# Optimization experiments

Hardware: AMD Instinct MI355X
Metric: run time of the kernel (lower is better)

Reference implementation:

```python
import jax, jax.numpy as jnp
import numpy as np

NUM_HEADS = 16
LN_EPS = 1e-5


def _layer_norm(x, w, b):
    mean = jnp.mean(x, axis=-1, keepdims=True)
    xc = x - mean
    var = jnp.mean(xc * xc, axis=-1, keepdims=True)
    return xc * jax.lax.rsqrt(var + LN_EPS) * w + b


def _triton_softmax(a):
    # Faithful to TritonSoftmax: clamp to [-100,100], stable softmax with
    # +1e-6 in the denominator, then +1e-8 and renormalize.
    a = jnp.clip(a, -100.0, 100.0)
    a = a - jnp.max(a, axis=-1, keepdims=True)
    e = jnp.exp(a)
    p = e / (jnp.sum(e, axis=-1, keepdims=True) + 1e-6)
    p = p + 1e-8
    return p / jnp.sum(p, axis=-1, keepdims=True)


def _triton_gelu(x):
    # y = 0.5*x*(1 + u/(1+|u|)) with u = x * sqrt(2/pi)*(1+0.044715*x^2)
    coeff = 0.7978845608028654 * (1.0 + 0.044715 * x * x)
    u = x * coeff
    return 0.5 * x * (1.0 + u / (1.0 + jnp.abs(u)))


def setup_inputs() -> dict:
    key = jax.random.key(0)
    ks = jax.random.split(key, 6)
    B, T, D = 2, 2048, 1024
    s = 0.02
    return {
        "x": jax.random.normal(ks[0], (B, T, D), jnp.float32),
        "ln1_w": jnp.ones((D,), jnp.float32),
        "ln1_b": jnp.zeros((D,), jnp.float32),
        "ln2_w": jnp.ones((D,), jnp.float32),
        "ln2_b": jnp.zeros((D,), jnp.float32),
        "w_qkv": jax.random.normal(ks[1], (D, 3 * D), jnp.float32) * s,
        "w_proj": jax.random.normal(ks[2], (D, D), jnp.float32) * s,
        "w_ff1": jax.random.normal(ks[3], (D, 4 * D), jnp.float32) * s,
        "w_ff2": jax.random.normal(ks[4], (4 * D, D), jnp.float32) * s,
    }


def reference(x, ln1_w, ln1_b, ln2_w, ln2_b, w_qkv, w_proj, w_ff1, w_ff2):
    B, T, D = x.shape
    H = NUM_HEADS
    hd = D // H
    scale = hd ** -0.5

    # ---- attention sublayer (pre-LN) ----
    h = _layer_norm(x, ln1_w, ln1_b)
    qkv = (h @ w_qkv).reshape(B, T, 3, H, hd).transpose(2, 0, 3, 1, 4)
    q, k, v = qkv[0], qkv[1], qkv[2]  # [B,H,T,hd]
    attn = jnp.einsum("bhqd,bhkd->bhqk", q, k) * scale  # [B,H,T,T]
    causal = jnp.tril(jnp.ones((T, T), bool))
    attn = jnp.where(causal, attn, -jnp.inf)
    attn = _triton_softmax(attn)  # dropout is identity at eval
    o = jnp.einsum("bhqk,bhkd->bhqd", attn, v)
    o = o.transpose(0, 2, 1, 3).reshape(B, T, D)
    x = x + o @ w_proj

    # ---- MLP sublayer (pre-LN) ----
    h = _layer_norm(x, ln2_w, ln2_b)
    x = x + _triton_gelu(h @ w_ff1) @ w_ff2
    return x
```

## Files before the change

kernel.cpp:

```cpp
#include <hip/hip_runtime.h>

typedef __attribute__((ext_vector_type(8))) __bf16 bf16x8;
typedef __attribute__((ext_vector_type(8))) unsigned short u16x8;
typedef __attribute__((ext_vector_type(4))) unsigned short u16x4;
typedef __attribute__((ext_vector_type(4))) float f32x4;

__device__ __forceinline__ unsigned short f2bf(float f) {
  return __builtin_bit_cast(unsigned short, (__bf16)f);
}

__device__ __forceinline__ bf16x8 ldb8(const unsigned short* p) {
  u16x8 u = *(const u16x8*)p;
  return __builtin_bit_cast(bf16x8, u);
}

__device__ __forceinline__ f32x4 mfma16(bf16x8 a, bf16x8 b, f32x4 c) {
  return __builtin_amdgcn_mfma_f32_16x16x32_bf16(a, b, c, 0, 0, 0);
}

__device__ __forceinline__ void gload16(const void* g, void* l) {
  __builtin_amdgcn_global_load_lds(
      (const __attribute__((address_space(1))) void*)g,
      (__attribute__((address_space(3))) void*)l, 16, 0, 0);
}

__device__ __forceinline__ float gelu_t(float x) {
  float u = x * (0.7978845608028654f * (1.0f + 0.044715f * x * x));
  return 0.5f * x * (1.0f + u / (1.0f + fabsf(u)));
}

__global__ __launch_bounds__(256) void tconv_kernel(const float* __restrict__ in,
                                                    unsigned short* __restrict__ out,
                                                    int R, int C) {
  __shared__ unsigned short tile[64][68];
  int r0 = blockIdx.y * 64, c0 = blockIdx.x * 64;
  int tx = threadIdx.x & 63, tg = threadIdx.x >> 6;
  for (int rr = tg; rr < 64; rr += 4)
    tile[tx][rr] = f2bf(in[(size_t)(r0 + rr) * C + c0 + tx]);
  __syncthreads();
  for (int cc = tg; cc < 64; cc += 4)
    out[(size_t)(c0 + cc) * R + r0 + tx] = tile[cc][tx];
}

__global__ __launch_bounds__(256) void vtrans_kernel(const unsigned short* __restrict__ V,
                                                     unsigned short* __restrict__ VT) {
  __shared__ unsigned short tile[64][68];
  int bh = blockIdx.y;
  int t0 = blockIdx.x * 64;
  const unsigned short* in = V + (size_t)bh * 2048 * 64;
  unsigned short* out = VT + (size_t)bh * 64 * 2048;
  int tx = threadIdx.x & 63, tg = threadIdx.x >> 6;
  for (int rr = tg; rr < 64; rr += 4)
    tile[tx][rr] = in[(size_t)(t0 + rr) * 64 + tx];
  __syncthreads();
  for (int dd = tg; dd < 64; dd += 4)
    out[(size_t)dd * 2048 + t0 + tx] = tile[dd][tx];
}

__global__ __launch_bounds__(256) void ln_kernel(const float* __restrict__ X,
                                                 const float* __restrict__ W,
                                                 const float* __restrict__ Bv,
                                                 unsigned short* __restrict__ H) {
  int row = blockIdx.x;
  int t = threadIdx.x;
  float4 v = ((const float4*)(X + (size_t)row * 1024))[t];
  float s = v.x + v.y + v.z + v.w;
  float s2 = v.x * v.x + v.y * v.y + v.z * v.z + v.w * v.w;
#pragma unroll
  for (int m = 32; m >= 1; m >>= 1) { s += __shfl_xor(s, m); s2 += __shfl_xor(s2, m); }
  __shared__ float red[8];
  if ((t & 63) == 0) { red[t >> 6] = s; red[4 + (t >> 6)] = s2; }
  __syncthreads();
  s = red[0] + red[1] + red[2] + red[3];
  s2 = red[4] + red[5] + red[6] + red[7];
  float mean = s * (1.f / 1024.f);
  float var = fmaxf(s2 * (1.f / 1024.f) - mean * mean, 0.f);
  float rs = rsqrtf(var + 1e-5f);
  float4 w4 = ((const float4*)W)[t];
  float4 b4 = ((const float4*)Bv)[t];
  u16x4 o;
  o[0] = f2bf((v.x - mean) * rs * w4.x + b4.x);
  o[1] = f2bf((v.y - mean) * rs * w4.y + b4.y);
  o[2] = f2bf((v.z - mean) * rs * w4.z + b4.z);
  o[3] = f2bf((v.w - mean) * rs * w4.w + b4.w);
  *(u16x4*)(H + (size_t)row * 1024 + t * 4) = o;
}

template <int MODE, bool DBUF>
__global__ __launch_bounds__(256) void gemm_kernel(
    const unsigned short* __restrict__ A, const unsigned short* __restrict__ B,
    const float* __restrict__ RES, void* __restrict__ OUT,
    unsigned short* __restrict__ Qo, unsigned short* __restrict__ Ko,
    unsigned short* __restrict__ Vo, int M, int N, int K) {
  __shared__ __align__(16) unsigned short As[DBUF ? 2 : 1][128 * 64];
  __shared__ __align__(16) unsigned short Bs[DBUF ? 2 : 1][128 * 64];
  const int tid = threadIdx.x;
  const int lane = tid & 63;
  const int wid = __builtin_amdgcn_readfirstlane(tid >> 6);
  const int lane16 = lane & 15, lgrp = lane >> 4;
  const int l8 = lane >> 3;
  const int lb = (lane & 7) * 16;
  const int m0 = blockIdx.y * 128, n0 = blockIdx.x * 128;
  const int wr = wid >> 1, wc = wid & 1;

  f32x4 acc[4][4] = {};

  const char* Ab = (const char*)A + (size_t)m0 * K * 2;
  const char* Bb = (const char*)B + (size_t)n0 * K * 2;
  const size_t rs = (size_t)K * 2;

  auto stage = [&](int k0, int b) {
#pragma unroll
    for (int i = 0; i < 4; ++i) {
      int c = wid * 4 + i;
      gload16(Ab + (size_t)(c * 8 + l8) * rs + (size_t)k0 * 2 + lb,
              (char*)&As[0][0] + b * 16384 + c * 1024);
      gload16(Bb + (size_t)(c * 8 + l8) * rs + (size_t)k0 * 2 + lb,
              (char*)&Bs[0][0] + b * 16384 + c * 1024);
    }
  };

  const int kIt = K / 64;
  if (DBUF) stage(0, 0);

  for (int it = 0; it < kIt; ++it) {
    int cur;
    if (DBUF) {
      cur = it & 1;
      asm volatile("s_waitcnt vmcnt(0)" ::: "memory");
      __syncthreads();
      if (it + 1 < kIt) stage((it + 1) * 64, cur ^ 1);
    } else {
      cur = 0;
      stage(it * 64, 0);
      asm volatile("s_waitcnt vmcnt(0)" ::: "memory");
      __syncthreads();
    }
#pragma unroll
    for (int ks = 0; ks < 2; ++ks) {
      bf16x8 af[4], bfr[4];
#pragma unroll
      for (int mf = 0; mf < 4; ++mf)
        af[mf] = ldb8(&As[cur][(wr * 64 + mf * 16 + lane16) * 64 + ks * 32 + lgrp * 8]);
#pragma unroll
      for (int nf = 0; nf < 4; ++nf)
        bfr[nf] = ldb8(&Bs[cur][(wc * 64 + nf * 16 + lane16) * 64 + ks * 32 + lgrp * 8]);
#pragma unroll
      for (int mf = 0; mf < 4; ++mf)
#pragma unroll
        for (int nf = 0; nf < 4; ++nf)
          acc[mf][nf] = mfma16(af[mf], bfr[nf], acc[mf][nf]);
    }
    if (!DBUF) __syncthreads();
  }

#pragma unroll
  for (int mf = 0; mf < 4; ++mf) {
    int row = m0 + wr * 64 + mf * 16 + lgrp * 4;
#pragma unroll
    for (int nf = 0; nf < 4; ++nf) {
      int col = n0 + wc * 64 + nf * 16 + lane16;
      if (MODE == 1) {
        float* o = (float*)OUT;
#pragma unroll
        for (int i = 0; i < 4; ++i) {
          size_t idx = (size_t)(row + i) * N + col;
          o[idx] = acc[mf][nf][i] + RES[idx];
        }
      } else if (MODE == 2) {
        unsigned short* o = (unsigned short*)OUT;
#pragma unroll
        for (int i = 0; i < 4; ++i)
          o[(size_t)(row + i) * N + col] = f2bf(gelu_t(acc[mf][nf][i]));
      } else {
        int bI = row >> 11, tI = row & 2047;
        unsigned short* dst;
        int dd;
        if (col < 1024) {
          dst = Qo + (size_t)(bI * 16 + (col >> 6)) * 2048 * 64;
          dd = col & 63;
        } else if (col < 2048) {
          int cc = col - 1024;
          dst = Ko + (size_t)(bI * 16 + (cc >> 6)) * 2048 * 64;
          dd = cc & 63;
        } else {
          int cc = col - 2048;
          dst = Vo + (size_t)(bI * 16 + (cc >> 6)) * 2048 * 64;
          dd = cc & 63;
        }
#pragma unroll
        for (int i = 0; i < 4; ++i)
          dst[(size_t)(tI + i) * 64 + dd] = f2bf(acc[mf][nf][i]);
      }
    }
  }
}

__global__ __launch_bounds__(256) void attn_kernel(const unsigned short* __restrict__ Q,
                                                   const unsigned short* __restrict__ Kb,
                                                   const unsigned short* __restrict__ VT,
                                                   unsigned short* __restrict__ O) {
  __shared__ __align__(16) unsigned short Ks[2][64 * 64];
  __shared__ __align__(16) unsigned short Vs[2][64 * 64];
  __shared__ __align__(16) unsigned short Ps[4][32 * 64];
  const int T = 2048;
  const int q0 = ((int)gridDim.x - 1 - (int)blockIdx.x) * 128;
  const int bh = blockIdx.y;
  const int tid = threadIdx.x, lane = tid & 63;
  const int wid = __builtin_amdgcn_readfirstlane(tid >> 6);
  const int lane16 = lane & 15, lgrp = lane >> 4;
  const int l8 = lane >> 3;
  const int swz = ((lane & 7) ^ (l8 & 7)) << 4;
  const float SCL2 = 0.18033688011112042f;

  const int qbase = q0 + wid * 32;
  bf16x8 qf[2][2];
#pragma unroll
  for (int qc = 0; qc < 2; ++qc) {
    const unsigned short* qp = Q + ((size_t)bh * T + qbase + qc * 16 + lane16) * 64;
    qf[qc][0] = ldb8(qp + lgrp * 8);
    qf[qc][1] = ldb8(qp + 32 + lgrp * 8);
  }

  const char* kg = (const char*)(Kb + (size_t)bh * T * 64);
  const char* vg = (const char*)(VT + (size_t)bh * 64 * T);
  char* PsB = (char*)&Ps[wid][0];

  auto stage = [&](int kv0, int b) {
#pragma unroll
    for (int i = 0; i < 2; ++i) {
      int c = wid * 2 + i;
      gload16(kg + (size_t)(kv0 + c * 8 + l8) * 128 + swz,
              (char*)&Ks[0][0] + b * 8192 + c * 1024);
      gload16(vg + (size_t)(c * 8 + l8) * (T * 2) + (size_t)kv0 * 2 + swz,
              (char*)&Vs[0][0] + b * 8192 + c * 1024);
    }
  };

  f32x4 acc_o[2][4] = {};
  float m_run[2] = {-1e30f, -1e30f};
  float l_run[2] = {0.f, 0.f};

  const int nkv = q0 / 64 + 2;
  stage(0, 0);
  for (int kt = 0; kt < nkv; ++kt) {
    const int kv0 = kt * 64;
    const int cur = kt & 1;
    asm volatile("s_waitcnt vmcnt(0)" ::: "memory");
    __syncthreads();
    if (kt + 1 < nkv) stage((kt + 1) * 64, cur ^ 1);

    const char* KsB = (const char*)&Ks[0][0] + cur * 8192;
    const char* VsB = (const char*)&Vs[0][0] + cur * 8192;

    bf16x8 kf[4][2], vf[4][2];
#pragma unroll
    for (int f = 0; f < 4; ++f)
#pragma unroll
      for (int c = 0; c < 2; ++c) {
        int row = f * 16 + lane16;
        int off = (c * 64 + lgrp * 16) ^ ((row & 7) << 4);
        kf[f][c] = ldb8((const unsigned short*)(KsB + row * 128 + off));
        vf[f][c] = ldb8((const unsigned short*)(VsB + row * 128 + off));
      }

#pragma unroll
    for (int qc = 0; qc < 2; ++qc) {
      const int qrow = qbase + qc * 16 + lane16;
      f32x4 accs[4] = {};
      __builtin_amdgcn_s_setprio(1);
#pragma unroll
      for (int kvf = 0; kvf < 4; ++kvf)
#pragma unroll
        for (int c = 0; c < 2; ++c)
          accs[kvf] = mfma16(kf[kvf][c], qf[qc][c], accs[kvf]);
      __builtin_amdgcn_s_setprio(0);

      float sc[16];
      if (kv0 + 64 <= qbase + qc * 16) {
#pragma unroll
        for (int kvf = 0; kvf < 4; ++kvf)
#pragma unroll
          for (int i = 0; i < 4; ++i)
            sc[kvf * 4 + i] = accs[kvf][i] * SCL2;
      } else {
#pragma unroll
        for (int kvf = 0; kvf < 4; ++kvf)
#pragma unroll
          for (int i = 0; i < 4; ++i) {
            int kv = kv0 + kvf * 16 + lgrp * 4 + i;
            float v = accs[kvf][i] * SCL2;
            sc[kvf * 4 + i] = (kv > qrow) ? -1e30f : v;
          }
      }
      float tmax = sc[0];
#pragma unroll
      for (int j = 1; j < 16; ++j) tmax = fmaxf(tmax, sc[j]);
      tmax = fmaxf(tmax, __shfl_xor(tmax, 16));
      tmax = fmaxf(tmax, __shfl_xor(tmax, 32));
      float m_c = m_run[qc];
      if (!__all(tmax <= m_c + 8.f)) {
        float m_new = fmaxf(m_c, tmax);
        float corr = exp2f(m_c - m_new);
        l_run[qc] *= corr;
        float cf0 = __shfl(corr, lgrp * 4 + 0);
        float cf1 = __shfl(corr, lgrp * 4 + 1);
        float cf2 = __shfl(corr, lgrp * 4 + 2);
        float cf3 = __shfl(corr, lgrp * 4 + 3);
#pragma unroll
        for (int df = 0; df < 4; ++df) {
          acc_o[qc][df][0] *= cf0; acc_o[qc][df][1] *= cf1;
          acc_o[qc][df][2] *= cf2; acc_o[qc][df][3] *= cf3;
        }
        m_run[qc] = m_new;
        m_c = m_new;
      }
      float p[16];
      float psum = 0.f;
#pragma unroll
      for (int j = 0; j < 16; ++j) { p[j] = exp2f(sc[j] - m_c); psum += p[j]; }
      psum += __shfl_xor(psum, 16);
      psum += __shfl_xor(psum, 32);
      l_run[qc] += psum;

      const int prow = qc * 16 + lane16;
#pragma unroll
      for (int kvf = 0; kvf < 4; ++kvf) {
        u16x4 pk;
#pragma unroll
        for (int i = 0; i < 4; ++i) pk[i] = f2bf(p[kvf * 4 + i]);
        *(u16x4*)(PsB + prow * 128 + ((kvf * 32 + lgrp * 8) ^ ((prow & 7) << 4))) = pk;
      }
      bf16x8 pf[2];
#pragma unroll
      for (int c = 0; c < 2; ++c)
        pf[c] = ldb8((const unsigned short*)(PsB + prow * 128 +
                     ((c * 64 + lgrp * 16) ^ ((prow & 7) << 4))));
      __builtin_amdgcn_s_setprio(1);
#pragma unroll
      for (int c = 0; c < 2; ++c)
#pragma unroll
        for (int df = 0; df < 4; ++df)
          acc_o[qc][df] = mfma16(pf[c], vf[df][c], acc_o[qc][df]);
      __builtin_amdgcn_s_setprio(0);
    }
  }

  const int b = bh >> 4, hh = bh & 15;
#pragma unroll
  for (int qc = 0; qc < 2; ++qc) {
    float il = 1.f / l_run[qc];
    float f0 = __shfl(il, lgrp * 4 + 0);
    float f1 = __shfl(il, lgrp * 4 + 1);
    float f2 = __shfl(il, lgrp * 4 + 2);
    float f3 = __shfl(il, lgrp * 4 + 3);
#pragma unroll
    for (int df = 0; df < 4; ++df) {
      int col = hh * 64 + df * 16 + lane16;
      size_t base = ((size_t)(b * T + qbase + qc * 16 + lgrp * 4)) * 1024 + col;
      O[base] = f2bf(acc_o[qc][df][0] * f0);
      O[base + 1024] = f2bf(acc_o[qc][df][1] * f1);
      O[base + 2048] = f2bf(acc_o[qc][df][2] * f2);
      O[base + 3072] = f2bf(acc_o[qc][df][3] * f3);
    }
  }
}

extern "C" void kernel_launch(void* const* d_in, const int* in_sizes, int n_in,
                              void* d_out, int out_size, void* d_ws, size_t ws_size,
                              hipStream_t stream) {
  (void)in_sizes; (void)n_in; (void)out_size; (void)ws_size;
  const float* x    = (const float*)d_in[0];
  const float* ln1w = (const float*)d_in[1];
  const float* ln1b = (const float*)d_in[2];
  const float* ln2w = (const float*)d_in[3];
  const float* ln2b = (const float*)d_in[4];
  const float* wqkv = (const float*)d_in[5];
  const float* wprj = (const float*)d_in[6];
  const float* wff1 = (const float*)d_in[7];
  const float* wff2 = (const float*)d_in[8];
  float* out = (float*)d_out;
  char* ws = (char*)d_ws;

  unsigned short* h      = (unsigned short*)(ws + 0);
  unsigned short* wqkvT  = (unsigned short*)(ws + 8388608);
  unsigned short* wprjT  = (unsigned short*)(ws + 14680064);
  unsigned short* wff1T  = (unsigned short*)(ws + 16777216);
  unsigned short* wff2T  = (unsigned short*)(ws + 25165824);
  unsigned short* qb     = (unsigned short*)(ws + 33554432);
  unsigned short* kb     = (unsigned short*)(ws + 41943040);
  unsigned short* vT     = (unsigned short*)(ws + 50331648);
  unsigned short* ob     = (unsigned short*)(ws + 58720256);
  unsigned short* h2     = (unsigned short*)(ws + 67108864);
  unsigned short* a1     = (unsigned short*)(ws + 75497472);
  unsigned short* vo     = h2;

  tconv_kernel<<<dim3(48, 16), 256, 0, stream>>>(wqkv, wqkvT, 1024, 3072);
  tconv_kernel<<<dim3(16, 16), 256, 0, stream>>>(wprj, wprjT, 1024, 1024);
  tconv_kernel<<<dim3(64, 16), 256, 0, stream>>>(wff1, wff1T, 1024, 4096);
  tconv_kernel<<<dim3(16, 64), 256, 0, stream>>>(wff2, wff2T, 4096, 1024);

  ln_kernel<<<4096, 256, 0, stream>>>(x, ln1w, ln1b, h);
  gemm_kernel<0, false><<<dim3(24, 32), 256, 0, stream>>>(h, wqkvT, nullptr, nullptr,
                                                          qb, kb, vo, 4096, 3072, 1024);
  vtrans_kernel<<<dim3(32, 32), 256, 0, stream>>>(vo, vT);
  attn_kernel<<<dim3(16, 32), 256, 0, stream>>>(qb, kb, vT, ob);
  gemm_kernel<1, true><<<dim3(8, 32), 256, 0, stream>>>(ob, wprjT, x, out,
                                                        nullptr, nullptr, nullptr, 4096, 1024, 1024);
  ln_kernel<<<4096, 256, 0, stream>>>(out, ln2w, ln2b, h2);
  gemm_kernel<2, false><<<dim3(32, 32), 256, 0, stream>>>(h2, wff1T, nullptr, a1,
                                                          nullptr, nullptr, nullptr, 4096, 4096, 1024);
  gemm_kernel<1, true><<<dim3(8, 32), 256, 0, stream>>>(a1, wff2T, out, out,
                                                        nullptr, nullptr, nullptr, 4096, 1024, 4096);
}
```

Before: 426.1 us.

## Shrink attention query tile to 64 and remap blocks for XCD locality and balance

Attention blocks now each cover 64 query rows (16 per wave) instead of 128, doubling the grid to 1024 blocks. A 1-D grid decodes blocks so each XCD handles four heads, with query tiles ordered in heavy/light pairs for causal load balance and L2 reuse of K/V. The aim is better occupancy, fewer idle CUs and shorter causal tail work. The cost is that K/V tiles are loaded twice as often per query row, and each wave now has less MFMA work per staged tile.

```diff
diff --git a/kernel.cpp b/kernel.cpp
--- a/kernel.cpp
+++ b/kernel.cpp
@@ -202,10 +202,15 @@
                                                    unsigned short* __restrict__ O) {
   __shared__ __align__(16) unsigned short Ks[2][64 * 64];
   __shared__ __align__(16) unsigned short Vs[2][64 * 64];
-  __shared__ __align__(16) unsigned short Ps[4][32 * 64];
+  __shared__ __align__(16) unsigned short Ps[4][16 * 64];
   const int T = 2048;
-  const int q0 = ((int)gridDim.x - 1 - (int)blockIdx.x) * 128;
-  const int bh = blockIdx.y;
+  const int lin = blockIdx.x;
+  const int xcd = lin & 7, idx = lin >> 3;
+  const int bh = (xcd << 2) + (idx >> 5);
+  const int j = idx & 31;
+  const int qt = (j & 1) ? (31 - (j >> 1)) : (j >> 1);
+  const int q0 = (31 - qt) * 64;
+
   const int tid = threadIdx.x, lane = tid & 63;
   const int wid = __builtin_amdgcn_readfirstlane(tid >> 6);
   const int lane16 = lane & 15, lgrp = lane >> 4;
@@ -213,14 +218,11 @@
   const int swz = ((lane & 7) ^ (l8 & 7)) << 4;
   const float SCL2 = 0.18033688011112042f;
 
-  const int qbase = q0 + wid * 32;
-  bf16x8 qf[2][2];
-#pragma unroll
-  for (int qc = 0; qc < 2; ++qc) {
-    const unsigned short* qp = Q + ((size_t)bh * T + qbase + qc * 16 + lane16) * 64;
-    qf[qc][0] = ldb8(qp + lgrp * 8);
-    qf[qc][1] = ldb8(qp + 32 + lgrp * 8);
-  }
+  const int qbase = q0 + wid * 16;
+  const unsigned short* qp = Q + ((size_t)bh * T + qbase + lane16) * 64;
+  bf16x8 qf[2];
+  qf[0] = ldb8(qp + lgrp * 8);
+  qf[1] = ldb8(qp + 32 + lgrp * 8);
 
   const char* kg = (const char*)(Kb + (size_t)bh * T * 64);
   const char* vg = (const char*)(VT + (size_t)bh * 64 * T);
@@ -237,11 +239,10 @@
     }
   };
 
-  f32x4 acc_o[2][4] = {};
-  float m_run[2] = {-1e30f, -1e30f};
-  float l_run[2] = {0.f, 0.f};
-
-  const int nkv = q0 / 64 + 2;
+  f32x4 acc_o[4] = {};
+  float m_run = -1e30f, l_run = 0.f;
+
+  const int nkv = q0 / 64 + 1;
   stage(0, 0);
   for (int kt = 0; kt < nkv; ++kt) {
     const int kv0 = kt * 64;
@@ -264,105 +265,99 @@
         vf[f][c] = ldb8((const unsigned short*)(VsB + row * 128 + off));
       }
 
-#pragma unroll
-    for (int qc = 0; qc < 2; ++qc) {
-      const int qrow = qbase + qc * 16 + lane16;
-      f32x4 accs[4] = {};
-      __builtin_amdgcn_s_setprio(1);
+    const int qrow = qbase + lane16;
+    f32x4 accs[4] = {};
+    __builtin_amdgcn_s_setprio(1);
+#pragma unroll
+    for (int kvf = 0; kvf < 4; ++kvf)
+#pragma unroll
+      for (int c = 0; c < 2; ++c)
+        accs[kvf] = mfma16(kf[kvf][c], qf[c], accs[kvf]);
+    __builtin_amdgcn_s_setprio(0);
+
+    float sc[16];
+    if (kv0 + 64 <= qbase) {
 #pragma unroll
       for (int kvf = 0; kvf < 4; ++kvf)
 #pragma unroll
-        for (int c = 0; c < 2; ++c)
-          accs[kvf] = mfma16(kf[kvf][c], qf[qc][c], accs[kvf]);
-      __builtin_amdgcn_s_setprio(0);
-
-      float sc[16];
-      if (kv0 + 64 <= qbase + qc * 16) {
-#pragma unroll
-        for (int kvf = 0; kvf < 4; ++kvf)
-#pragma unroll
-          for (int i = 0; i < 4; ++i)
-            sc[kvf * 4 + i] = accs[kvf][i] * SCL2;
-      } else {
-#pragma unroll
-        for (int kvf = 0; kvf < 4; ++kvf)
-#pragma unroll
-          for (int i = 0; i < 4; ++i) {
-            int kv = kv0 + kvf * 16 + lgrp * 4 + i;
-            float v = accs[kvf][i] * SCL2;
-            sc[kvf * 4 + i] = (kv > qrow) ? -1e30f : v;
-          }
+        for (int i = 0; i < 4; ++i)
+          sc[kvf * 4 + i] = accs[kvf][i] * SCL2;
+    } else {
+#pragma unroll
+      for (int kvf = 0; kvf < 4; ++kvf)
+#pragma unroll
+        for (int i = 0; i < 4; ++i) {
+          int kv = kv0 + kvf * 16 + lgrp * 4 + i;
+          float v = accs[kvf][i] * SCL2;
+          sc[kvf * 4 + i] = (kv > qrow) ? -1e30f : v;
+        }
+    }
+    float tmax = sc[0];
+#pragma unroll
+    for (int jj = 1; jj < 16; ++jj) tmax = fmaxf(tmax, sc[jj]);
+    tmax = fmaxf(tmax, __shfl_xor(tmax, 16));
+    tmax = fmaxf(tmax, __shfl_xor(tmax, 32));
+    float m_c = m_run;
+    if (!__all(tmax <= m_c + 8.f)) {
+      float m_new = fmaxf(m_c, tmax);
+      float corr = exp2f(m_c - m_new);
+      l_run *= corr;
+      float cf0 = __shfl(corr, lgrp * 4 + 0);
+      float cf1 = __shfl(corr, lgrp * 4 + 1);
+      float cf2 = __shfl(corr, lgrp * 4 + 2);
+      float cf3 = __shfl(corr, lgrp * 4 + 3);
+#pragma unroll
+      for (int df = 0; df < 4; ++df) {
+        acc_o[df][0] *= cf0; acc_o[df][1] *= cf1;
+        acc_o[df][2] *= cf2; acc_o[df][3] *= cf3;
       }
-      float tmax = sc[0];
-#pragma unroll
-      for (int j = 1; j < 16; ++j) tmax = fmaxf(tmax, sc[j]);
-      tmax = fmaxf(tmax, __shfl_xor(tmax, 16));
-      tmax = fmaxf(tmax, __shfl_xor(tmax, 32));
-      float m_c = m_run[qc];
-      if (!__all(tmax <= m_c + 8.f)) {
-        float m_new = fmaxf(m_c, tmax);
-        float corr = exp2f(m_c - m_new);
-        l_run[qc] *= corr;
-        float cf0 = __shfl(corr, lgrp * 4 + 0);
-        float cf1 = __shfl(corr, lgrp * 4 + 1);
-        float cf2 = __shfl(corr, lgrp * 4 + 2);
-        float cf3 = __shfl(corr, lgrp * 4 + 3);
-#pragma unroll
-        for (int df = 0; df < 4; ++df) {
-          acc_o[qc][df][0] *= cf0; acc_o[qc][df][1] *= cf1;
-          acc_o[qc][df][2] *= cf2; acc_o[qc][df][3] *= cf3;
-        }
-        m_run[qc] = m_new;
-        m_c = m_new;
-      }
-      float p[16];
-      float psum = 0.f;
-#pragma unroll
-      for (int j = 0; j < 16; ++j) { p[j] = exp2f(sc[j] - m_c); psum += p[j]; }
-      psum += __shfl_xor(psum, 16);
-      psum += __shfl_xor(psum, 32);
-      l_run[qc] += psum;
-
-      const int prow = qc * 16 + lane16;
-#pragma unroll
-      for (int kvf = 0; kvf < 4; ++kvf) {
-        u16x4 pk;
-#pragma unroll
-        for (int i = 0; i < 4; ++i) pk[i] = f2bf(p[kvf * 4 + i]);
-        *(u16x4*)(PsB + prow * 128 + ((kvf * 32 + lgrp * 8) ^ ((prow & 7) << 4))) = pk;
-      }
-      bf16x8 pf[2];
-#pragma unroll
-      for (int c = 0; c < 2; ++c)
-        pf[c] = ldb8((const unsigned short*)(PsB + prow * 128 +
-                     ((c * 64 + lgrp * 16) ^ ((prow & 7) << 4))));
-      __builtin_amdgcn_s_setprio(1);
-#pragma unroll
-      for (int c = 0; c < 2; ++c)
-#pragma unroll
-        for (int df = 0; df < 4; ++df)
-          acc_o[qc][df] = mfma16(pf[c], vf[df][c], acc_o[qc][df]);
-      __builtin_amdgcn_s_setprio(0);
-    }
+      m_run = m_new;
+      m_c = m_new;
+    }
+    float p[16];
+    float psum = 0.f;
+#pragma unroll
+    for (int jj = 0; jj < 16; ++jj) { p[jj] = exp2f(sc[jj] - m_c); psum += p[jj]; }
+    psum += __shfl_xor(psum, 16);
+    psum += __shfl_xor(psum, 32);
+    l_run += psum;
+
+    const int prow = lane16;
+#pragma unroll
+    for (int kvf = 0; kvf < 4; ++kvf) {
+      u16x4 pk;
+#pragma unroll
+      for (int i = 0; i < 4; ++i) pk[i] = f2bf(p[kvf * 4 + i]);
+      *(u16x4*)(PsB + prow * 128 + ((kvf * 32 + lgrp * 8) ^ ((prow & 7) << 4))) = pk;
+    }
+    bf16x8 pf[2];
+#pragma unroll
+    for (int c = 0; c < 2; ++c)
+      pf[c] = ldb8((const unsigned short*)(PsB + prow * 128 +
+                   ((c * 64 + lgrp * 16) ^ ((prow & 7) << 4))));
+    __builtin_amdgcn_s_setprio(1);
+#pragma unroll
+    for (int c = 0; c < 2; ++c)
+#pragma unroll
+      for (int df = 0; df < 4; ++df)
+        acc_o[df] = mfma16(pf[c], vf[df][c], acc_o[df]);
+    __builtin_amdgcn_s_setprio(0);
   }
 
   const int b = bh >> 4, hh = bh & 15;
-#pragma unroll
-  for (int qc = 0; qc < 2; ++qc) {
-    float il = 1.f / l_run[qc];
-    float f0 = __shfl(il, lgrp * 4 + 0);
-    float f1 = __shfl(il, lgrp * 4 + 1);
-    float f2 = __shfl(il, lgrp * 4 + 2);
-    float f3 = __shfl(il, lgrp * 4 + 3);
-#pragma unroll
-    for (int df = 0; df < 4; ++df) {
-      int col = hh * 64 + df * 16 + lane16;
-      size_t base = ((size_t)(b * T + qbase + qc * 16 + lgrp * 4)) * 1024 + col;
-      O[base] = f2bf(acc_o[qc][df][0] * f0);
-      O[base + 1024] = f2bf(acc_o[qc][df][1] * f1);
-      O[base + 2048] = f2bf(acc_o[qc][df][2] * f2);
-      O[base + 3072] = f2bf(acc_o[qc][df][3] * f3);
-    }
+  float il = 1.f / l_run;
+  float f0 = __shfl(il, lgrp * 4 + 0);
+  float f1 = __shfl(il, lgrp * 4 + 1);
+  float f2 = __shfl(il, lgrp * 4 + 2);
+  float f3 = __shfl(il, lgrp * 4 + 3);
+#pragma unroll
+  for (int df = 0; df < 4; ++df) {
+    int col = hh * 64 + df * 16 + lane16;
+    size_t base = ((size_t)(b * T + qbase + lgrp * 4)) * 1024 + col;
+    O[base] = f2bf(acc_o[df][0] * f0);
+    O[base + 1024] = f2bf(acc_o[df][1] * f1);
+    O[base + 2048] = f2bf(acc_o[df][2] * f2);
+    O[base + 3072] = f2bf(acc_o[df][3] * f3);
   }
 }
 
@@ -404,7 +399,7 @@
   gemm_kernel<0, false><<<dim3(24, 32), 256, 0, stream>>>(h, wqkvT, nullptr, nullptr,
                                                           qb, kb, vo, 4096, 3072, 1024);
   vtrans_kernel<<<dim3(32, 32), 256, 0, stream>>>(vo, vT);
-  attn_kernel<<<dim3(16, 32), 256, 0, stream>>>(qb, kb, vT, ob);
+  attn_kernel<<<1024, 256, 0, stream>>>(qb, kb, vT, ob);
   gemm_kernel<1, true><<<dim3(8, 32), 256, 0, stream>>>(ob, wprjT, x, out,
                                                         nullptr, nullptr, nullptr, 4096, 1024, 1024);
   ln_kernel<<<4096, 256, 0, stream>>>(out, ln2w, ln2b, h2);
```

New measurement: 417.5 us. 1.02x faster.
